# Performance work log

Measured on AMD Instinct MI355X. Metric: run time of the kernel, lower is better.

## Reference

```python
import jax, jax.numpy as jnp
import numpy as np

N = 100000      # nodes
DEG = 16        # fixed out-degree per row of adj
E = N * DEG     # edges
IN_F, H_F, OUT_F = 64, 64, 64


def setup_inputs() -> dict:
    key = jax.random.key(0)
    k1, k2, k3, k4, k5, k6 = jax.random.split(key, 6)
    x = jax.random.normal(k1, (N, IN_F), dtype=jnp.float32)
    # fixed-degree graph: row i of adj has exactly DEG neighbors -> rowsum = DEG > 0
    dst = jnp.repeat(jnp.arange(N, dtype=jnp.int32), DEG)          # [E]
    src = jax.random.randint(k2, (E,), 0, N, dtype=jnp.int32)       # [E]
    # Linear params (torch nn.Linear: y = x @ W.T + b); store as [in, out]
    s1 = 1.0 / np.sqrt(2 * IN_F)
    s2 = 1.0 / np.sqrt(2 * H_F)
    W1 = jax.random.uniform(k3, (2 * IN_F, H_F), jnp.float32, -s1, s1)
    b1 = jax.random.uniform(k4, (H_F,), jnp.float32, -s1, s1)
    W2 = jax.random.uniform(k5, (2 * H_F, OUT_F), jnp.float32, -s2, s2)
    b2 = jax.random.uniform(k6, (OUT_F,), jnp.float32, -s2, s2)
    return {"x": x, "W1": W1, "b1": b1, "W2": W2, "b2": b2, "src": src, "dst": dst}


def _spmm_mean(h, src, dst, n_nodes):
    # row-normalized sparse adj @ h  == mean over neighbors (rows have DEG nbrs)
    deg = jax.ops.segment_sum(jnp.ones_like(src, dtype=h.dtype), dst, num_segments=n_nodes)
    w = (1.0 / jnp.maximum(deg, 1.0))[dst]                 # [E] edge weights 1/rowsum
    return jax.ops.segment_sum(h[src] * w[:, None], dst, num_segments=n_nodes)


def reference(x, W1, b1, W2, b2, src, dst):
    n = x.shape[0]
    h_neigh = _spmm_mean(x, src, dst, n)                   # [N, in]
    h = jnp.concatenate([x, h_neigh], axis=1)              # [N, 2*in]
    h = jax.nn.relu(h @ W1 + b1)                           # [N, h]
    h_neigh2 = _spmm_mean(h, src, dst, n)                  # [N, h]
    h2 = jnp.concatenate([h, h_neigh2], axis=1)            # [N, 2*h]
    return h2 @ W2 + b2                                    # [N, out]
```

## Files before the change

kernel.cpp:

```cpp
#include <hip/hip_runtime.h>


#define NN   100000
#define DEG  16
#define F    64
#define NPB  64
#define STR  65
#define JPW  16
#define EDG  (NN * DEG)

#if __has_builtin(__builtin_amdgcn_cvt_pk_f32_fp8) && __has_builtin(__builtin_amdgcn_cvt_pk_fp8_f32)
#define HW_FP8 1
#else
#define HW_FP8 0
#endif

typedef float v2f __attribute__((ext_vector_type(2)));

__device__ __forceinline__ ushort f2bf(float f) {
    unsigned u = __float_as_uint(f);
    return (ushort)((u + 0x7fffu + ((u >> 16) & 1u)) >> 16);
}
__device__ __forceinline__ float bf2f(ushort u) {
    return __uint_as_float(((unsigned)u) << 16);
}

#if !HW_FP8
__device__ __forceinline__ unsigned fp8_enc1(float f) {
    const unsigned u = __float_as_uint(f);
    const unsigned s = (u >> 31) << 7;
    const float af = fabsf(f);
    if (!(af < 448.f)) return s | 0x7E;
    if (af < 0.015625f) {
        const int n = (int)rintf(af * 512.f);
        return s | (unsigned)n;
    }
    unsigned au = u & 0x7FFFFFFFu;
    const unsigned lsb = (au >> 20) & 1u;
    au += 0x7FFFFu + lsb;
    const int e = (int)(au >> 23) - 127;
    if (e > 8) return s | 0x7E;
    return s | ((unsigned)(e + 7) << 3) | ((au >> 20) & 7u);
}
__device__ __forceinline__ float fp8_dec1(unsigned c) {
    const unsigned s = c >> 7;
    const int e = (int)((c >> 3) & 15u);
    const unsigned m = c & 7u;
    const float v = e ? ldexpf((float)(8 + m), e - 10) : ldexpf((float)m, -9);
    return s ? -v : v;
}
#endif

__device__ __forceinline__ unsigned fp8_pack4(float a, float b, float c, float d) {
#if HW_FP8
    int t = __builtin_amdgcn_cvt_pk_fp8_f32(a, b, 0, false);
    t     = __builtin_amdgcn_cvt_pk_fp8_f32(c, d, t, true);
    return (unsigned)t;
#else
    return fp8_enc1(a) | (fp8_enc1(b) << 8) | (fp8_enc1(c) << 16) | (fp8_enc1(d) << 24);
#endif
}

__device__ __forceinline__ void fp8_acc4(unsigned d, float* acc) {
#if HW_FP8
    const v2f lo = __builtin_amdgcn_cvt_pk_f32_fp8((int)d, false);
    const v2f hi = __builtin_amdgcn_cvt_pk_f32_fp8((int)d, true);
    acc[0] += lo.x; acc[1] += lo.y; acc[2] += hi.x; acc[3] += hi.y;
#else
    acc[0] += fp8_dec1(d & 0xffu);
    acc[1] += fp8_dec1((d >> 8) & 0xffu);
    acc[2] += fp8_dec1((d >> 16) & 0xffu);
    acc[3] += fp8_dec1(d >> 24);
#endif
}

__global__ __launch_bounds__(256)
void cvt_f32_fp8(const float* __restrict__ in, unsigned* __restrict__ out, int n4)
{
    int i = blockIdx.x * 256 + threadIdx.x;
    if (i < n4) {
        float4 v = ((const float4*)in)[i];
        out[i] = fp8_pack4(v.x, v.y, v.z, v.w);
    }
}

__device__ __forceinline__ void ce(unsigned& a, unsigned& b) {
    const unsigned lo = min(a, b), hi = max(a, b); a = lo; b = hi;
}
__device__ __forceinline__ void sort16(unsigned s[16]) {
    #pragma unroll
    for (int p = 1; p < 16; p <<= 1) {
        #pragma unroll
        for (int k = p; k >= 1; k >>= 1) {
            #pragma unroll
            for (int j = k & (p - 1); j + k < 16; j += 2 * k) {
                #pragma unroll
                for (int i = 0; i < k; ++i) {
                    if (i + j + k < 16)
                        if ((i + j) / (2 * p) == (i + j + k) / (2 * p))
                            ce(s[i + j], s[i + j + k]);
                }
            }
        }
    }
}

template<bool RELU, bool SELF_F32, bool EMIT_F32>
__global__ __launch_bounds__(256, 4)
void sage_fused(const float*  __restrict__ selfA,
                const ushort* __restrict__ selfB,
                const unsigned char* __restrict__ gat,
                const float*  __restrict__ W,
                const float*  __restrict__ bias,
                const int*    __restrict__ src,
                float*        __restrict__ out_f32,
                ushort*       __restrict__ out_bf16,
                unsigned char* __restrict__ out_fp8)
{
    __shared__ float    bufA[F][STR];
    __shared__ unsigned bufB[F / 2][STR];

    const int tid   = threadIdx.x;
    const int lane  = tid & 63;
    const int wave  = __builtin_amdgcn_readfirstlane(tid >> 6);
    const int node0 = blockIdx.x * NPB;

    if (SELF_F32) {
        #pragma unroll
        for (int m = 0; m < 4; ++m) {
            const int i    = m * 256 + tid;
            const int n    = i >> 4;
            const int fq   = i & 15;
            const int node = node0 + n;
            float4 v = make_float4(0.f, 0.f, 0.f, 0.f);
            if (node < NN)
                v = *(const float4*)(selfA + (size_t)node * F + fq * 4);
            bufA[fq * 4 + 0][n] = v.x;
            bufA[fq * 4 + 1][n] = v.y;
            bufA[fq * 4 + 2][n] = v.z;
            bufA[fq * 4 + 3][n] = v.w;
        }
    } else {
        #pragma unroll
        for (int m = 0; m < 2; ++m) {
            const int i    = m * 256 + tid;
            const int n    = i >> 3;
            const int oc   = i & 7;
            const int node = node0 + n;
            uint4 v = make_uint4(0u, 0u, 0u, 0u);
            if (node < NN)
                v = *(const uint4*)(selfB + (size_t)node * F + oc * 8);
            #pragma unroll
            for (int t = 0; t < 4; ++t) {
                const unsigned d = (&v.x)[t];
                bufA[oc * 8 + 2 * t    ][n] = __uint_as_float(d << 16);
                bufA[oc * 8 + 2 * t + 1][n] = __uint_as_float(d & 0xffff0000u);
            }
        }
    }

    {
        const int q     = lane & 3;
        const int g     = lane >> 2;
        const int nloc  = wave * JPW + g;
        const int n     = node0 + nloc;
        const bool v    = n < NN;

        unsigned s[DEG];
        {
            const int4* p = (const int4*)(src + (size_t)n * DEG);
            #pragma unroll
            for (int t = 0; t < 4; ++t) {
                const int4 a = v ? p[t] : make_int4(0, 0, 0, 0);
                s[4*t+0] = a.x; s[4*t+1] = a.y;
                s[4*t+2] = a.z; s[4*t+3] = a.w;
            }
        }
        sort16(s);

        float a[16];
        #pragma unroll
        for (int f = 0; f < 16; ++f) a[f] = 0.f;

        #pragma unroll
        for (int e = 0; e < DEG; ++e) {
            const uint4 r = *(const uint4*)(gat + (size_t)s[e] * F + q * 16);
            fp8_acc4(r.x, a);
            fp8_acc4(r.y, a + 4);
            fp8_acc4(r.z, a + 8);
            fp8_acc4(r.w, a + 12);
        }

        #pragma unroll
        for (int t = 0; t < 8; ++t) {
            const unsigned d =
                (unsigned)f2bf(a[2*t]     * (1.0f / DEG)) |
                ((unsigned)f2bf(a[2*t+1]  * (1.0f / DEG)) << 16);
            bufB[8 * q + t][nloc] = d;
        }
    }
    __syncthreads();

    const int j0 = wave * JPW;
    float acc[JPW];
    #pragma unroll
    for (int j = 0; j < JPW; ++j) acc[j] = bias[j0 + j];

    #pragma unroll 4
    for (int k = 0; k < F; ++k) {
        const float v = bufA[k][lane];
        const float* Wr = W + k * F + j0;
        #pragma unroll
        for (int j = 0; j < JPW; ++j)
            acc[j] = fmaf(v, Wr[j], acc[j]);
    }
    #pragma unroll 2
    for (int kk = 0; kk < F / 2; ++kk) {
        const unsigned d = bufB[kk][lane];
        const float vlo = __uint_as_float(d << 16);
        const float vhi = __uint_as_float(d & 0xffff0000u);
        const float* Wlo = W + (F + 2 * kk)     * F + j0;
        const float* Whi = W + (F + 2 * kk + 1) * F + j0;
        #pragma unroll
        for (int j = 0; j < JPW; ++j) {
            acc[j] = fmaf(vlo, Wlo[j], acc[j]);
            acc[j] = fmaf(vhi, Whi[j], acc[j]);
        }
    }

    const int node = node0 + lane;
    if (node < NN) {
        if (RELU) {
            #pragma unroll
            for (int j = 0; j < JPW; ++j) acc[j] = fmaxf(acc[j], 0.f);
        }
        if (EMIT_F32) {
            float4* op = (float4*)(out_f32 + (size_t)node * F + j0);
            #pragma unroll
            for (int t = 0; t < 4; ++t)
                op[t] = make_float4(acc[4 * t], acc[4 * t + 1],
                                    acc[4 * t + 2], acc[4 * t + 3]);
        } else {
            uint4 q0, q1;
            #pragma unroll
            for (int t = 0; t < 8; ++t)
                (t < 4 ? (&q0.x)[t] : (&q1.x)[t - 4]) =
                    (unsigned)f2bf(acc[2 * t]) |
                    ((unsigned)f2bf(acc[2 * t + 1]) << 16);
            uint4* ob = (uint4*)(out_bf16 + (size_t)node * F + j0);
            ob[0] = q0; ob[1] = q1;

            uint4 p;
            #pragma unroll
            for (int t = 0; t < 4; ++t)
                (&p.x)[t] = fp8_pack4(acc[4*t], acc[4*t+1], acc[4*t+2], acc[4*t+3]);
            *(uint4*)(out_fp8 + (size_t)node * F + j0) = p;
        }
    }
}

template<bool RELU>
__global__ __launch_bounds__(256, 4)
void sage_layer_f32(const float* __restrict__ feat,
                    const float* __restrict__ W,
                    const float* __restrict__ bias,
                    const int*   __restrict__ src,
                    float*       __restrict__ out)
{
    __shared__ float buf[2 * F][STR];
    const int tid   = threadIdx.x;
    const int lane  = tid & 63;
    const int wave  = __builtin_amdgcn_readfirstlane(tid >> 6);
    const int node0 = blockIdx.x * NPB;

    #pragma unroll 2
    for (int m = 0; m < NPB / 4; ++m) {
        const int n    = wave * (NPB / 4) + m;
        const int node = node0 + n;
        if (node < NN) {
            buf[lane][n] = feat[node * F + lane];
            const int* sp = src + node * DEG;
            float s = 0.f;
            #pragma unroll
            for (int e = 0; e < DEG; ++e) s += feat[sp[e] * F + lane];
            buf[F + lane][n] = s * (1.0f / DEG);
        }
    }
    __syncthreads();

    const int j0 = wave * JPW;
    float acc[JPW];
    #pragma unroll
    for (int j = 0; j < JPW; ++j) acc[j] = bias[j0 + j];
    #pragma unroll 4
    for (int k = 0; k < 2 * F; ++k) {
        const float v = buf[k][lane];
        const float* Wr = W + k * F + j0;
        #pragma unroll
        for (int j = 0; j < JPW; ++j) acc[j] = fmaf(v, Wr[j], acc[j]);
    }
    const int node = node0 + lane;
    if (node < NN) {
        float4* op = (float4*)(out + node * F + j0);
        #pragma unroll
        for (int t = 0; t < 4; ++t) {
            float4 r = make_float4(acc[4 * t], acc[4 * t + 1],
                                   acc[4 * t + 2], acc[4 * t + 3]);
            if (RELU) {
                r.x = fmaxf(r.x, 0.f); r.y = fmaxf(r.y, 0.f);
                r.z = fmaxf(r.z, 0.f); r.w = fmaxf(r.w, 0.f);
            }
            op[t] = r;
        }
    }
}

extern "C" void kernel_launch(void* const* d_in, const int* in_sizes, int n_in,
                              void* d_out, int out_size, void* d_ws, size_t ws_size,
                              hipStream_t stream) {
    const float* x   = (const float*)d_in[0];
    const float* W1  = (const float*)d_in[1];
    const float* b1  = (const float*)d_in[2];
    const float* W2  = (const float*)d_in[3];
    const float* b2  = (const float*)d_in[4];
    const int*   src = (const int*)d_in[5];

    float* out = (float*)d_out;
    const int blocks = (NN + NPB - 1) / NPB;

    const size_t hFP8 = (size_t)NN * F;
    const size_t hBF  = (size_t)NN * F * sizeof(ushort);

    if (ws_size >= 2 * hFP8 + hBF) {
        unsigned char* x_fp8 = (unsigned char*)d_ws;
        ushort*        h_bf  = (ushort*)((char*)d_ws + hFP8);
        unsigned char* h_fp8 = (unsigned char*)d_ws + hFP8 + hBF;

        const int n4 = NN * F / 4;
        cvt_f32_fp8<<<(n4 + 255) / 256, 256, 0, stream>>>(x, (unsigned*)x_fp8, n4);
        sage_fused<true,  true,  false><<<blocks, 256, 0, stream>>>(
            x, nullptr, x_fp8, W1, b1, src, nullptr, h_bf, h_fp8);
        sage_fused<false, false, true ><<<blocks, 256, 0, stream>>>(
            nullptr, h_bf, h_fp8, W2, b2, src, out, nullptr, nullptr);
    } else {
        float* h = (float*)d_ws;
        sage_layer_f32<true ><<<blocks, 256, 0, stream>>>(x, W1, b1, src, h);
        sage_layer_f32<false><<<blocks, 256, 0, stream>>>(h, W2, b2, src, out);
    }
}
```

Baseline: 164.4 us.

## Store intermediates as packed fp16 in LDS and use packed f32x2 FMAs

Replaces the bf16 intermediate and the fp32 self-feature LDS tile with packed fp16 pairs, halving LDS use for the self tile. The dense matmul now accumulates into f32x2 vectors via elementwise FMA so the compiler can emit packed FMA instructions. This aims to cut LDS footprint and traffic and to roughly halve the FMA instruction count. It adds fp16 conversion cost and range risk: the x self features are now rounded to fp16, which loses precision relative to fp32.

```diff
diff --git a/kernel.cpp b/kernel.cpp
--- a/kernel.cpp
+++ b/kernel.cpp
@@ -15,14 +15,19 @@
 #define HW_FP8 0
 #endif
 
-typedef float v2f __attribute__((ext_vector_type(2)));
-
-__device__ __forceinline__ ushort f2bf(float f) {
-    unsigned u = __float_as_uint(f);
-    return (ushort)((u + 0x7fffu + ((u >> 16) & 1u)) >> 16);
-}
-__device__ __forceinline__ float bf2f(ushort u) {
-    return __uint_as_float(((unsigned)u) << 16);
+typedef float v2f  __attribute__((ext_vector_type(2)));
+typedef float f32x2 __attribute__((ext_vector_type(2)));
+
+__device__ __forceinline__ unsigned pkh(float a, float b) {
+    union { _Float16 h[2]; unsigned u; } t;
+    t.h[0] = (_Float16)a; t.h[1] = (_Float16)b;
+    return t.u;
+}
+__device__ __forceinline__ float h_lo(unsigned d) {
+    union { unsigned u; _Float16 h[2]; } t; t.u = d; return (float)t.h[0];
+}
+__device__ __forceinline__ float h_hi(unsigned d) {
+    union { unsigned u; _Float16 h[2]; } t; t.u = d; return (float)t.h[1];
 }
 
 #if !HW_FP8
@@ -108,17 +113,17 @@
 template<bool RELU, bool SELF_F32, bool EMIT_F32>
 __global__ __launch_bounds__(256, 4)
 void sage_fused(const float*  __restrict__ selfA,
-                const ushort* __restrict__ selfB,
+                const ushort* __restrict__ selfH,
                 const unsigned char* __restrict__ gat,
                 const float*  __restrict__ W,
                 const float*  __restrict__ bias,
                 const int*    __restrict__ src,
                 float*        __restrict__ out_f32,
-                ushort*       __restrict__ out_bf16,
+                ushort*       __restrict__ out_h16,
                 unsigned char* __restrict__ out_fp8)
 {
-    __shared__ float    bufA[F][STR];
-    __shared__ unsigned bufB[F / 2][STR];
+    __shared__ unsigned pkA[F / 2][STR];
+    __shared__ unsigned pkB[F / 2][STR];
 
     const int tid   = threadIdx.x;
     const int lane  = tid & 63;
@@ -135,10 +140,8 @@
             float4 v = make_float4(0.f, 0.f, 0.f, 0.f);
             if (node < NN)
                 v = *(const float4*)(selfA + (size_t)node * F + fq * 4);
-            bufA[fq * 4 + 0][n] = v.x;
-            bufA[fq * 4 + 1][n] = v.y;
-            bufA[fq * 4 + 2][n] = v.z;
-            bufA[fq * 4 + 3][n] = v.w;
+            pkA[2 * fq    ][n] = pkh(v.x, v.y);
+            pkA[2 * fq + 1][n] = pkh(v.z, v.w);
         }
     } else {
         #pragma unroll
@@ -149,13 +152,11 @@
             const int node = node0 + n;
             uint4 v = make_uint4(0u, 0u, 0u, 0u);
             if (node < NN)
-                v = *(const uint4*)(selfB + (size_t)node * F + oc * 8);
-            #pragma unroll
-            for (int t = 0; t < 4; ++t) {
-                const unsigned d = (&v.x)[t];
-                bufA[oc * 8 + 2 * t    ][n] = __uint_as_float(d << 16);
-                bufA[oc * 8 + 2 * t + 1][n] = __uint_as_float(d & 0xffff0000u);
-            }
+                v = *(const uint4*)(selfH + (size_t)node * F + oc * 8);
+            pkA[4 * oc + 0][n] = v.x;
+            pkA[4 * oc + 1][n] = v.y;
+            pkA[4 * oc + 2][n] = v.z;
+            pkA[4 * oc + 3][n] = v.w;
         }
     }
 
@@ -191,69 +192,74 @@
             fp8_acc4(r.w, a + 12);
         }
 
+        const float sc = 1.0f / DEG;
+        #pragma unroll
+        for (int t = 0; t < 8; ++t)
+            pkB[8 * q + t][nloc] = pkh(a[2*t] * sc, a[2*t+1] * sc);
+    }
+    __syncthreads();
+
+    const int j0 = wave * JPW;
+    f32x2 acc2[8];
+    #pragma unroll
+    for (int t = 0; t < 8; ++t)
+        acc2[t] = *(const f32x2*)(bias + j0 + 2 * t);
+
+    #pragma unroll 4
+    for (int kk = 0; kk < F / 2; ++kk) {
+        const unsigned d = pkA[kk][lane];
+        const float vlo = h_lo(d), vhi = h_hi(d);
+        const float* Wl = W + (2 * kk)     * F + j0;
+        const float* Wh = W + (2 * kk + 1) * F + j0;
         #pragma unroll
         for (int t = 0; t < 8; ++t) {
-            const unsigned d =
-                (unsigned)f2bf(a[2*t]     * (1.0f / DEG)) |
-                ((unsigned)f2bf(a[2*t+1]  * (1.0f / DEG)) << 16);
-            bufB[8 * q + t][nloc] = d;
-        }
-    }
-    __syncthreads();
-
-    const int j0 = wave * JPW;
-    float acc[JPW];
-    #pragma unroll
-    for (int j = 0; j < JPW; ++j) acc[j] = bias[j0 + j];
-
+            acc2[t] = __builtin_elementwise_fma((f32x2){vlo, vlo},
+                        *(const f32x2*)(Wl + 2 * t), acc2[t]);
+            acc2[t] = __builtin_elementwise_fma((f32x2){vhi, vhi},
+                        *(const f32x2*)(Wh + 2 * t), acc2[t]);
+        }
+    }
     #pragma unroll 4
-    for (int k = 0; k < F; ++k) {
-        const float v = bufA[k][lane];
-        const float* Wr = W + k * F + j0;
-        #pragma unroll
-        for (int j = 0; j < JPW; ++j)
-            acc[j] = fmaf(v, Wr[j], acc[j]);
-    }
-    #pragma unroll 2
     for (int kk = 0; kk < F / 2; ++kk) {
-        const unsigned d = bufB[kk][lane];
-        const float vlo = __uint_as_float(d << 16);
-        const float vhi = __uint_as_float(d & 0xffff0000u);
-        const float* Wlo = W + (F + 2 * kk)     * F + j0;
-        const float* Whi = W + (F + 2 * kk + 1) * F + j0;
-        #pragma unroll
-        for (int j = 0; j < JPW; ++j) {
-            acc[j] = fmaf(vlo, Wlo[j], acc[j]);
-            acc[j] = fmaf(vhi, Whi[j], acc[j]);
+        const unsigned d = pkB[kk][lane];
+        const float vlo = h_lo(d), vhi = h_hi(d);
+        const float* Wl = W + (F + 2 * kk)     * F + j0;
+        const float* Wh = W + (F + 2 * kk + 1) * F + j0;
+        #pragma unroll
+        for (int t = 0; t < 8; ++t) {
+            acc2[t] = __builtin_elementwise_fma((f32x2){vlo, vlo},
+                        *(const f32x2*)(Wl + 2 * t), acc2[t]);
+            acc2[t] = __builtin_elementwise_fma((f32x2){vhi, vhi},
+                        *(const f32x2*)(Wh + 2 * t), acc2[t]);
         }
     }
 
     const int node = node0 + lane;
     if (node < NN) {
-        if (RELU) {
-            #pragma unroll
-            for (int j = 0; j < JPW; ++j) acc[j] = fmaxf(acc[j], 0.f);
+        float r[JPW];
+        #pragma unroll
+        for (int t = 0; t < 8; ++t) {
+            r[2*t]   = RELU ? fmaxf(acc2[t][0], 0.f) : acc2[t][0];
+            r[2*t+1] = RELU ? fmaxf(acc2[t][1], 0.f) : acc2[t][1];
         }
         if (EMIT_F32) {
             float4* op = (float4*)(out_f32 + (size_t)node * F + j0);
             #pragma unroll
             for (int t = 0; t < 4; ++t)
-                op[t] = make_float4(acc[4 * t], acc[4 * t + 1],
-                                    acc[4 * t + 2], acc[4 * t + 3]);
+                op[t] = make_float4(r[4 * t], r[4 * t + 1],
+                                    r[4 * t + 2], r[4 * t + 3]);
         } else {
             uint4 q0, q1;
             #pragma unroll
             for (int t = 0; t < 8; ++t)
-                (t < 4 ? (&q0.x)[t] : (&q1.x)[t - 4]) =
-                    (unsigned)f2bf(acc[2 * t]) |
-                    ((unsigned)f2bf(acc[2 * t + 1]) << 16);
-            uint4* ob = (uint4*)(out_bf16 + (size_t)node * F + j0);
+                (t < 4 ? (&q0.x)[t] : (&q1.x)[t - 4]) = pkh(r[2*t], r[2*t+1]);
+            uint4* ob = (uint4*)(out_h16 + (size_t)node * F + j0);
             ob[0] = q0; ob[1] = q1;
 
             uint4 p;
             #pragma unroll
             for (int t = 0; t < 4; ++t)
-                (&p.x)[t] = fp8_pack4(acc[4*t], acc[4*t+1], acc[4*t+2], acc[4*t+3]);
+                (&p.x)[t] = fp8_pack4(r[4*t], r[4*t+1], r[4*t+2], r[4*t+3]);
             *(uint4*)(out_fp8 + (size_t)node * F + j0) = p;
         }
     }
@@ -329,19 +335,19 @@
     const int blocks = (NN + NPB - 1) / NPB;
 
     const size_t hFP8 = (size_t)NN * F;
-    const size_t hBF  = (size_t)NN * F * sizeof(ushort);
-
-    if (ws_size >= 2 * hFP8 + hBF) {
+    const size_t hF16 = (size_t)NN * F * sizeof(ushort);
+
+    if (ws_size >= 2 * hFP8 + hF16) {
         unsigned char* x_fp8 = (unsigned char*)d_ws;
-        ushort*        h_bf  = (ushort*)((char*)d_ws + hFP8);
-        unsigned char* h_fp8 = (unsigned char*)d_ws + hFP8 + hBF;
+        ushort*        h_16  = (ushort*)((char*)d_ws + hFP8);
+        unsigned char* h_fp8 = (unsigned char*)d_ws + hFP8 + hF16;
 
         const int n4 = NN * F / 4;
         cvt_f32_fp8<<<(n4 + 255) / 256, 256, 0, stream>>>(x, (unsigned*)x_fp8, n4);
         sage_fused<true,  true,  false><<<blocks, 256, 0, stream>>>(
-            x, nullptr, x_fp8, W1, b1, src, nullptr, h_bf, h_fp8);
+            x, nullptr, x_fp8, W1, b1, src, nullptr, h_16, h_fp8);
         sage_fused<false, false, true ><<<blocks, 256, 0, stream>>>(
-            nullptr, h_bf, h_fp8, W2, b2, src, out, nullptr, nullptr);
+            nullptr, h_16, h_fp8, W2, b2, src, out, nullptr, nullptr);
     } else {
         float* h = (float*)d_ws;
         sage_layer_f32<true ><<<blocks, 256, 0, stream>>>(x, W1, b1, src, h);
```

Result: faster. 159.4 us (-3.0%).
